# Kernel optimization log

Hardware: AMD Instinct MI355X
Metric: run time of the kernel (lower is better)

## Reference

```python
import jax, jax.numpy as jnp
import numpy as np

N_CLASSES = 4
N_FEATURES = 13
N_HIDDEN = 13
N_STEPS = 100
FORGET_BIAS = 1.0


def setup_inputs() -> dict:
    key = jax.random.key(0)
    ks = jax.random.split(key, 10)
    B = 32768
    return {
        "x_input": jax.random.normal(ks[0], (B, N_STEPS, N_FEATURES), dtype=jnp.float32),
        # input projection (tf.random.normal mean=0.5 in original; values irrelevant for correctness test)
        "w_hidden": jax.random.normal(ks[1], (N_FEATURES, N_HIDDEN), dtype=jnp.float32) * 0.5 + 0.5,
        "b_hidden": jax.random.normal(ks[2], (N_HIDDEN,), dtype=jnp.float32) * 0.5 + 0.5,
        # BasicLSTMCell params: kernel [input_dim + hidden, 4*hidden], gate order (i, j, f, o)
        "lstm0_kernel": jax.random.normal(ks[3], (N_HIDDEN + N_HIDDEN, 4 * N_HIDDEN), dtype=jnp.float32) * 0.2,
        "lstm0_bias": jnp.zeros((4 * N_HIDDEN,), dtype=jnp.float32),
        "lstm1_kernel": jax.random.normal(ks[4], (N_HIDDEN + N_HIDDEN, 4 * N_HIDDEN), dtype=jnp.float32) * 0.2,
        "lstm1_bias": jnp.zeros((4 * N_HIDDEN,), dtype=jnp.float32),
        "w_output": jax.random.normal(ks[5], (N_HIDDEN, N_CLASSES), dtype=jnp.float32) * 0.5 + 0.5,
        "b_output": jax.random.normal(ks[6], (N_CLASSES,), dtype=jnp.float32) * 0.5 + 0.5,
    }


def _lstm_cell(x, c, h, kernel, bias):
    # BasicLSTMCell: z = [x; h] @ W + b, split -> i, j, f, o
    z = jnp.concatenate([x, h], axis=-1) @ kernel + bias
    i, j, f, o = jnp.split(z, 4, axis=-1)
    c_new = c * jax.nn.sigmoid(f + FORGET_BIAS) + jax.nn.sigmoid(i) * jnp.tanh(j)
    h_new = jnp.tanh(c_new) * jax.nn.sigmoid(o)
    return c_new, h_new


def reference(x_input, w_hidden, b_hidden, lstm0_kernel, lstm0_bias,
              lstm1_kernel, lstm1_bias, w_output, b_output):
    B = x_input.shape[0]
    # input projection + relu, batched over all timesteps: [B,T,F] -> [T,B,H]
    hidden = jax.nn.relu(jnp.einsum('btf,fh->bth', x_input, w_hidden) + b_hidden)
    hidden = jnp.transpose(hidden, (1, 0, 2))  # [T, B, H]

    zeros = jnp.zeros((B, N_HIDDEN), dtype=x_input.dtype)
    init = (zeros, zeros, zeros, zeros)  # (c0, h0, c1, h1)

    def step(carry, x_t):
        c0, h0, c1, h1 = carry
        c0, h0 = _lstm_cell(x_t, c0, h0, lstm0_kernel, lstm0_bias)
        c1, h1 = _lstm_cell(h0, c1, h1, lstm1_kernel, lstm1_bias)
        return (c0, h0, c1, h1), None

    (c0, h0, c1, h1), _ = jax.lax.scan(step, init, hidden)
    # last output of top LSTM layer -> output projection
    return h1 @ w_output + b_output
```

## Files before the change

kernel.cpp:

```cpp
#include <hip/hip_runtime.h>
#include <cstdint>

typedef __bf16          bf16x8 __attribute__((ext_vector_type(8)));
typedef float           f32x4  __attribute__((ext_vector_type(4)));
typedef unsigned short  u16x8  __attribute__((ext_vector_type(8)));

#define MFMA16(a,b,c) __builtin_amdgcn_mfma_f32_16x16x32_bf16((a),(b),(c),0,0,0)

__device__ __forceinline__ float rcpf(float x) { return __builtin_amdgcn_rcpf(x); }
__device__ __forceinline__ float ex2(float x)  { return __builtin_amdgcn_exp2f(x); }

__device__ __forceinline__ void split2(float v, unsigned short& hi, unsigned short& lo) {
    unsigned u = __builtin_bit_cast(unsigned, v);
    hi = (unsigned short)(u >> 16);
    float rem = v - __builtin_bit_cast(float, u & 0xffff0000u);
    lo = (unsigned short)(__builtin_bit_cast(unsigned, rem) >> 16);
}
__device__ __forceinline__ __bf16 bfbits(unsigned short b) { return __builtin_bit_cast(__bf16, b); }


constexpr float KL = 1.4426950408889634f;

__global__ __launch_bounds__(256, 4)
void lstm_fused(const float* __restrict__ x,
                const float* __restrict__ w_hidden,
                const float* __restrict__ b_hidden,
                const float* __restrict__ k0,
                const float* __restrict__ b0,
                const float* __restrict__ k1,
                const float* __restrict__ b1,
                const float* __restrict__ w_out,
                const float* __restrict__ b_out,
                float* __restrict__ out)
{
    __shared__ __attribute__((aligned(16))) unsigned short xh_s[2][2][2][384];
    __shared__ __attribute__((aligned(16))) unsigned short h0_s[2][2][2][384];
    __shared__ __attribute__((aligned(16))) unsigned short h1_s[2][2][384];

    const int lane = threadIdx.x & 63;
    const int wv   = threadIdx.x >> 6;
    const int grp  = wv >> 1;
    const int role = wv & 1;
    const int col  = lane & 15;
    const int q    = lane >> 4;
    const int qh   = q & 1;
    const int s0   = (blockIdx.x * 2 + grp) * 16;

    {
        unsigned short* a0 = &xh_s[0][0][0][0];
        unsigned short* a1 = &h0_s[0][0][0][0];
        for (int idx = threadIdx.x; idx < 3072; idx += 256) {
            unsigned short v = ((idx % 24) == 13 && ((idx / 384) & 1) == 0)
                             ? (unsigned short)0x3F80 : (unsigned short)0;
            a0[idx] = v; a1[idx] = v;
        }
        unsigned short* a2 = &h1_s[0][0][0];
        for (int idx = threadIdx.x; idx < 1536; idx += 256) {
            unsigned short v = ((idx % 24) == 13 && ((idx / 384) & 1) == 0)
                             ? (unsigned short)0x3F80 : (unsigned short)0;
            a2[idx] = v;
        }
    }

    const float* kp = role ? k1 : k0;
    const float* bb = role ? b1 : b0;
    bf16x8 Kh[4], Kl[4];
    #pragma unroll
    for (int g = 0; g < 4; ++g) {
        bf16x8 hv{}, lv{};
        #pragma unroll
        for (int j = 0; j < 8; ++j) {
            int k = 8 * q + j;
            float w = 0.f;
            if (col < 13) {
                if (k < 13)                 w = kp[k * 52 + 13 * g + col];
                else if (k == 13)           w = bb[13 * g + col] + (g == 2 ? 1.f : 0.f);
                else if (k >= 16 && k < 29) w = kp[(13 + k - 16) * 52 + 13 * g + col];
            }
            unsigned short h_, l_;
            split2(w, h_, l_);
            hv[j] = bfbits(h_); lv[j] = bfbits(l_);
        }
        Kh[g] = hv; Kl[g] = lv;
    }

    bf16x8 Ph{}, Pl{};
    if (role) {
        #pragma unroll
        for (int j = 0; j < 8; ++j) {
            int k = 8 * q + j;
            float w = 0.f;
            if (col < 13) {
                if (k < 13)       w = w_hidden[k * 13 + col];
                else if (k == 13) w = b_hidden[col];
            }
            unsigned short h_, l_;
            split2(w, h_, l_);
            Ph[j] = bfbits(h_); Pl[j] = bfbits(l_);
        }
    }

    const float* xrow = x + (size_t)(s0 + col) * 1300;

    auto elem = [&](float zi, float zj, float zf, float zo, float& c) -> float {
        float a   = ex2(-KL * zi);
        float b   = ex2(-2.f * KL * zj);
        float fe  = ex2(-KL * zf);
        float g   = ex2(-KL * zo);
        float opa = 1.f + a, opb = 1.f + b, opf = 1.f + fe;
        float pab = opa * opb;
        float r1  = rcpf(pab * opf);
        float cn  = fmaf(c, pab, (1.f - b) * opf) * r1;
        c = cn;
        float d   = ex2(-2.f * KL * cn);
        float r2  = rcpf((1.f + d) * (1.f + g));
        return (1.f - d) * r2;
    };

    auto cell = [&](const unsigned short* inH, const unsigned short* hidH,
                    unsigned short* outH, float* cst) {
        const unsigned short* pA = (q < 2) ? inH : hidH;
        bf16x8 ah = __builtin_bit_cast(bf16x8, *(const u16x8*)(pA + col * 24 + 8 * qh));
        bf16x8 al = __builtin_bit_cast(bf16x8, *(const u16x8*)(pA + 384 + col * 24 + 8 * qh));
        f32x4 z0 = {0.f,0.f,0.f,0.f}, z1 = z0, z2 = z0, z3 = z0;
        z0 = MFMA16(ah, Kh[0], z0); z0 = MFMA16(al, Kh[0], z0); z0 = MFMA16(ah, Kl[0], z0);
        z1 = MFMA16(ah, Kh[1], z1); z1 = MFMA16(al, Kh[1], z1); z1 = MFMA16(ah, Kl[1], z1);
        z2 = MFMA16(ah, Kh[2], z2); z2 = MFMA16(al, Kh[2], z2); z2 = MFMA16(ah, Kl[2], z2);
        z3 = MFMA16(ah, Kh[3], z3); z3 = MFMA16(al, Kh[3], z3); z3 = MFMA16(ah, Kl[3], z3);
        #pragma unroll
        for (int r = 0; r < 4; ++r) {
            float hv = elem(z0[r], z1[r], z2[r], z3[r], cst[r]);
            unsigned short hh, hl;
            split2(hv, hh, hl);
            if (col < 13) {
                outH[(4 * q + r) * 24 + col]       = hh;
                outH[384 + (4 * q + r) * 24 + col] = hl;
            }
        }
    };

    auto proj = [&](int t, unsigned short* oH) {
        bf16x8 axh{}, axl{};
        if (q < 2) {
            const float* p = xrow + t * 13;
            #pragma unroll
            for (int j = 0; j < 8; ++j) {
                int k  = 8 * q + j;
                int kk = k > 12 ? 12 : k;
                float v = p[kk];
                if (k > 12) v = 0.f;
                unsigned short h_, l_;
                split2(v, h_, l_);
                axh[j] = bfbits(h_); axl[j] = bfbits(l_);
            }
            if (q == 1) { axh[5] = bfbits(0x3F80); axl[5] = bfbits(0); }
        }
        f32x4 zp = {0.f,0.f,0.f,0.f};
        zp = MFMA16(axh, Ph, zp);
        zp = MFMA16(axl, Ph, zp);
        zp = MFMA16(axh, Pl, zp);
        #pragma unroll
        for (int r = 0; r < 4; ++r) {
            float v = fmaxf(zp[r], 0.f);
            unsigned short hh, hl;
            split2(v, hh, hl);
            if (col < 13) {
                oH[(4 * q + r) * 24 + col]       = hh;
                oH[384 + (4 * q + r) * 24 + col] = hl;
            }
        }
    };

    float cst[4] = {0.f, 0.f, 0.f, 0.f};

    __syncthreads();
    if (role) proj(0, &xh_s[grp][0][0][0]);
    __syncthreads();

    for (int i = 0; i <= 100; ++i) {
        int p = i & 1;
        if (role == 0) {
            if (i < 100)
                cell(&xh_s[grp][p][0][0], &h0_s[grp][p ^ 1][0][0],
                     &h0_s[grp][p][0][0], cst);
        } else {
            if (i >= 1)
                cell(&h0_s[grp][p ^ 1][0][0], &h1_s[grp][0][0],
                     &h1_s[grp][0][0], cst);
            if (i < 99) proj(i + 1, &xh_s[grp][p ^ 1][0][0]);
        }
        __syncthreads();
    }

    if (role) {
        bf16x8 Oh{}, Ol{};
        #pragma unroll
        for (int j = 0; j < 8; ++j) {
            int k = 8 * q + j;
            float w = 0.f;
            if (col < 4) {
                if (k < 13)       w = w_out[k * 4 + col];
                else if (k == 13) w = b_out[col];
            }
            unsigned short h_, l_;
            split2(w, h_, l_);
            Oh[j] = bfbits(h_); Ol[j] = bfbits(l_);
        }
        const unsigned short* pA = &h1_s[grp][0][0];
        bf16x8 ah = __builtin_bit_cast(bf16x8, *(const u16x8*)(pA + col * 24 + 8 * qh));
        bf16x8 al = __builtin_bit_cast(bf16x8, *(const u16x8*)(pA + 384 + col * 24 + 8 * qh));
        f32x4 zf = {0.f,0.f,0.f,0.f};
        zf = MFMA16(ah, Oh, zf);
        zf = MFMA16(al, Oh, zf);
        zf = MFMA16(ah, Ol, zf);
        if (col < 4) {
            #pragma unroll
            for (int r = 0; r < 4; ++r)
                out[(size_t)(s0 + 4 * q + r) * 4 + col] = zf[r];
        }
    }
}

extern "C" void kernel_launch(void* const* d_in, const int* in_sizes, int n_in,
                              void* d_out, int out_size, void* d_ws, size_t ws_size,
                              hipStream_t stream) {
    (void)in_sizes; (void)n_in; (void)d_ws; (void)ws_size; (void)out_size;
    lstm_fused<<<dim3(1024), dim3(256), 0, stream>>>(
        (const float*)d_in[0], (const float*)d_in[1], (const float*)d_in[2],
        (const float*)d_in[3], (const float*)d_in[4], (const float*)d_in[5],
        (const float*)d_in[6], (const float*)d_in[7], (const float*)d_in[8],
        (float*)d_out);
}
```

Measured before the change: 372.5 us.

## Split input projection onto a dedicated third wave per group

Each block now runs three waves per 16-sample group instead of two: one for layer 0, one for layer 1, and a new one for the input projection and ReLU, which previously shared a wave with layer 1. This shortens the critical path of each barrier-separated step, since layer 1 no longer also does the projection. The projection wave reuses the Kh registers for its weights, MFMA chains now start from a shared zero accumulator, and launch bounds move to 384 threads with 6 blocks per CU. The cost is 50% more waves per block, which can raise register pressure and add barrier participants.

```diff
diff --git a/kernel.cpp b/kernel.cpp
--- a/kernel.cpp
+++ b/kernel.cpp
@@ -21,7 +21,7 @@
 
 constexpr float KL = 1.4426950408889634f;
 
-__global__ __launch_bounds__(256, 4)
+__global__ __launch_bounds__(384, 6)
 void lstm_fused(const float* __restrict__ x,
                 const float* __restrict__ w_hidden,
                 const float* __restrict__ b_hidden,
@@ -39,8 +39,8 @@
 
     const int lane = threadIdx.x & 63;
     const int wv   = threadIdx.x >> 6;
-    const int grp  = wv >> 1;
-    const int role = wv & 1;
+    const int grp  = wv / 3;
+    const int role = wv % 3;
     const int col  = lane & 15;
     const int q    = lane >> 4;
     const int qh   = q & 1;
@@ -49,43 +49,43 @@
     {
         unsigned short* a0 = &xh_s[0][0][0][0];
         unsigned short* a1 = &h0_s[0][0][0][0];
-        for (int idx = threadIdx.x; idx < 3072; idx += 256) {
+        for (int idx = threadIdx.x; idx < 3072; idx += 384) {
             unsigned short v = ((idx % 24) == 13 && ((idx / 384) & 1) == 0)
                              ? (unsigned short)0x3F80 : (unsigned short)0;
             a0[idx] = v; a1[idx] = v;
         }
         unsigned short* a2 = &h1_s[0][0][0];
-        for (int idx = threadIdx.x; idx < 1536; idx += 256) {
+        for (int idx = threadIdx.x; idx < 1536; idx += 384) {
             unsigned short v = ((idx % 24) == 13 && ((idx / 384) & 1) == 0)
                              ? (unsigned short)0x3F80 : (unsigned short)0;
             a2[idx] = v;
         }
     }
 
-    const float* kp = role ? k1 : k0;
-    const float* bb = role ? b1 : b0;
     bf16x8 Kh[4], Kl[4];
-    #pragma unroll
-    for (int g = 0; g < 4; ++g) {
+    if (role < 2) {
+        const float* kp = role ? k1 : k0;
+        const float* bb = role ? b1 : b0;
+        #pragma unroll
+        for (int g = 0; g < 4; ++g) {
+            bf16x8 hv{}, lv{};
+            #pragma unroll
+            for (int j = 0; j < 8; ++j) {
+                int k = 8 * q + j;
+                float w = 0.f;
+                if (col < 13) {
+                    if (k < 13)                 w = kp[k * 52 + 13 * g + col];
+                    else if (k == 13)           w = bb[13 * g + col] + (g == 2 ? 1.f : 0.f);
+                    else if (k >= 16 && k < 29) w = kp[(13 + k - 16) * 52 + 13 * g + col];
+                }
+                unsigned short h_, l_;
+                split2(w, h_, l_);
+                hv[j] = bfbits(h_); lv[j] = bfbits(l_);
+            }
+            Kh[g] = hv; Kl[g] = lv;
+        }
+    } else {
         bf16x8 hv{}, lv{};
-        #pragma unroll
-        for (int j = 0; j < 8; ++j) {
-            int k = 8 * q + j;
-            float w = 0.f;
-            if (col < 13) {
-                if (k < 13)                 w = kp[k * 52 + 13 * g + col];
-                else if (k == 13)           w = bb[13 * g + col] + (g == 2 ? 1.f : 0.f);
-                else if (k >= 16 && k < 29) w = kp[(13 + k - 16) * 52 + 13 * g + col];
-            }
-            unsigned short h_, l_;
-            split2(w, h_, l_);
-            hv[j] = bfbits(h_); lv[j] = bfbits(l_);
-        }
-        Kh[g] = hv; Kl[g] = lv;
-    }
-
-    bf16x8 Ph{}, Pl{};
-    if (role) {
         #pragma unroll
         for (int j = 0; j < 8; ++j) {
             int k = 8 * q + j;
@@ -96,11 +96,14 @@
             }
             unsigned short h_, l_;
             split2(w, h_, l_);
-            Ph[j] = bfbits(h_); Pl[j] = bfbits(l_);
-        }
+            hv[j] = bfbits(h_); lv[j] = bfbits(l_);
+        }
+        Kh[0] = hv; Kh[1] = lv;
     }
 
     const float* xrow = x + (size_t)(s0 + col) * 1300;
+
+    const f32x4 Z4 = {0.f, 0.f, 0.f, 0.f};
 
     auto elem = [&](float zi, float zj, float zf, float zo, float& c) -> float {
         float a   = ex2(-KL * zi);
@@ -122,11 +125,14 @@
         const unsigned short* pA = (q < 2) ? inH : hidH;
         bf16x8 ah = __builtin_bit_cast(bf16x8, *(const u16x8*)(pA + col * 24 + 8 * qh));
         bf16x8 al = __builtin_bit_cast(bf16x8, *(const u16x8*)(pA + 384 + col * 24 + 8 * qh));
-        f32x4 z0 = {0.f,0.f,0.f,0.f}, z1 = z0, z2 = z0, z3 = z0;
-        z0 = MFMA16(ah, Kh[0], z0); z0 = MFMA16(al, Kh[0], z0); z0 = MFMA16(ah, Kl[0], z0);
-        z1 = MFMA16(ah, Kh[1], z1); z1 = MFMA16(al, Kh[1], z1); z1 = MFMA16(ah, Kl[1], z1);
-        z2 = MFMA16(ah, Kh[2], z2); z2 = MFMA16(al, Kh[2], z2); z2 = MFMA16(ah, Kl[2], z2);
-        z3 = MFMA16(ah, Kh[3], z3); z3 = MFMA16(al, Kh[3], z3); z3 = MFMA16(ah, Kl[3], z3);
+        f32x4 z0 = MFMA16(ah, Kh[0], Z4);
+        f32x4 z1 = MFMA16(ah, Kh[1], Z4);
+        f32x4 z2 = MFMA16(ah, Kh[2], Z4);
+        f32x4 z3 = MFMA16(ah, Kh[3], Z4);
+        z0 = MFMA16(al, Kh[0], z0); z0 = MFMA16(ah, Kl[0], z0);
+        z1 = MFMA16(al, Kh[1], z1); z1 = MFMA16(ah, Kl[1], z1);
+        z2 = MFMA16(al, Kh[2], z2); z2 = MFMA16(ah, Kl[2], z2);
+        z3 = MFMA16(al, Kh[3], z3); z3 = MFMA16(ah, Kl[3], z3);
         #pragma unroll
         for (int r = 0; r < 4; ++r) {
             float hv = elem(z0[r], z1[r], z2[r], z3[r], cst[r]);
@@ -155,10 +161,9 @@
             }
             if (q == 1) { axh[5] = bfbits(0x3F80); axl[5] = bfbits(0); }
         }
-        f32x4 zp = {0.f,0.f,0.f,0.f};
-        zp = MFMA16(axh, Ph, zp);
-        zp = MFMA16(axl, Ph, zp);
-        zp = MFMA16(axh, Pl, zp);
+        f32x4 zp = MFMA16(axh, Kh[0], Z4);
+        zp = MFMA16(axl, Kh[0], zp);
+        zp = MFMA16(axh, Kh[1], zp);
         #pragma unroll
         for (int r = 0; r < 4; ++r) {
             float v = fmaxf(zp[r], 0.f);
@@ -174,7 +179,7 @@
     float cst[4] = {0.f, 0.f, 0.f, 0.f};
 
     __syncthreads();
-    if (role) proj(0, &xh_s[grp][0][0][0]);
+    if (role == 2) proj(0, &xh_s[grp][0][0][0]);
     __syncthreads();
 
     for (int i = 0; i <= 100; ++i) {
@@ -183,16 +188,17 @@
             if (i < 100)
                 cell(&xh_s[grp][p][0][0], &h0_s[grp][p ^ 1][0][0],
                      &h0_s[grp][p][0][0], cst);
-        } else {
+        } else if (role == 1) {
             if (i >= 1)
                 cell(&h0_s[grp][p ^ 1][0][0], &h1_s[grp][0][0],
                      &h1_s[grp][0][0], cst);
+        } else {
             if (i < 99) proj(i + 1, &xh_s[grp][p ^ 1][0][0]);
         }
         __syncthreads();
     }
 
-    if (role) {
+    if (role == 1) {
         bf16x8 Oh{}, Ol{};
         #pragma unroll
         for (int j = 0; j < 8; ++j) {
@@ -209,8 +215,7 @@
         const unsigned short* pA = &h1_s[grp][0][0];
         bf16x8 ah = __builtin_bit_cast(bf16x8, *(const u16x8*)(pA + col * 24 + 8 * qh));
         bf16x8 al = __builtin_bit_cast(bf16x8, *(const u16x8*)(pA + 384 + col * 24 + 8 * qh));
-        f32x4 zf = {0.f,0.f,0.f,0.f};
-        zf = MFMA16(ah, Oh, zf);
+        f32x4 zf = MFMA16(ah, Oh, Z4);
         zf = MFMA16(al, Oh, zf);
         zf = MFMA16(ah, Ol, zf);
         if (col < 4) {
@@ -225,7 +230,7 @@
                               void* d_out, int out_size, void* d_ws, size_t ws_size,
                               hipStream_t stream) {
     (void)in_sizes; (void)n_in; (void)d_ws; (void)ws_size; (void)out_size;
-    lstm_fused<<<dim3(1024), dim3(256), 0, stream>>>(
+    lstm_fused<<<dim3(1024), dim3(384), 0, stream>>>(
         (const float*)d_in[0], (const float*)d_in[1], (const float*)d_in[2],
         (const float*)d_in[3], (const float*)d_in[4], (const float*)d_in[5],
         (const float*)d_in[6], (const float*)d_in[7], (const float*)d_in[8],
```

New measurement: 442.7 us. 1.19x slower.
